# Kernel optimization log

Measured on AMD Instinct MI355X. Metric: run time of the kernel, lower is better.

Reference implementation:

```python
import jax, jax.numpy as jnp
import numpy as np

HIDDEN = 1024
HEADS = 16
HEAD_DIM = HIDDEN // HEADS


def setup_inputs() -> dict:
    key = jax.random.key(0)
    ks = jax.random.split(key, 9)
    s = 1.0 / np.sqrt(HIDDEN)
    inp = {
        "x": jax.random.normal(ks[0], (2, 2048, HIDDEN), dtype=jnp.float32),
        "Wq": jax.random.uniform(ks[1], (HIDDEN, HIDDEN), jnp.float32, -s, s),
        "bq": jax.random.uniform(ks[2], (HIDDEN,), jnp.float32, -s, s),
        "Wk": jax.random.uniform(ks[3], (HIDDEN, HIDDEN), jnp.float32, -s, s),
        "bk": jax.random.uniform(ks[4], (HIDDEN,), jnp.float32, -s, s),
        "Wv": jax.random.uniform(ks[5], (HIDDEN, HIDDEN), jnp.float32, -s, s),
        "bv": jax.random.uniform(ks[6], (HIDDEN,), jnp.float32, -s, s),
        "Wo": jax.random.uniform(ks[7], (HIDDEN, HIDDEN), jnp.float32, -s, s),
        "bo": jax.random.uniform(ks[8], (HIDDEN,), jnp.float32, -s, s),
    }
    return inp


def reference(x, Wq, bq, Wk, bk, Wv, bv, Wo, bo):
    B, S, _ = x.shape
    # QKV projections; reshape to [B, H, S, D]
    def heads(t):
        return t.reshape(B, S, HEADS, HEAD_DIM).transpose(0, 2, 1, 3)
    q = heads(x @ Wq + bq)
    k = heads(x @ Wk + bk)
    v = heads(x @ Wv + bv)
    scale = 1.0 / np.sqrt(HEAD_DIM)
    scores = jnp.einsum('bhqd,bhkd->bhqk', q, k) * scale  # [B,H,S,S]
    attn = jax.nn.softmax(scores, axis=-1)
    out = jnp.einsum('bhqk,bhkd->bhqd', attn, v)  # [B,H,S,D]
    out = out.transpose(0, 2, 1, 3).reshape(B, S, HIDDEN)
    return out @ Wo + bo
```

## Files before the change

kernel.cpp:

```cpp
#include <hip/hip_runtime.h>
#include <math.h>


namespace {

constexpr int kHID = 1024;
constexpr int kNH  = 16;
constexpr int kHD  = 64;
constexpr int kSEQ = 2048;

constexpr float kQScale = 0.125f * 1.4426950408889634f;

typedef unsigned short ushortT;
typedef __attribute__((ext_vector_type(8))) short   bf16x8;
typedef __attribute__((ext_vector_type(4))) float   f32x4;
typedef __attribute__((ext_vector_type(4))) unsigned short u16x4;

#define MFMA(a, b, c) __builtin_amdgcn_mfma_f32_16x16x32_bf16((a), (b), (c), 0, 0, 0)
#define SBAR() __builtin_amdgcn_s_barrier()
#define WAITV0() asm volatile("s_waitcnt vmcnt(0)" ::: "memory")
#define WAITV3() asm volatile("s_waitcnt vmcnt(3)" ::: "memory")
#define WAITV4() asm volatile("s_waitcnt vmcnt(4)" ::: "memory")

typedef const __attribute__((address_space(1))) void GVoid;
typedef __attribute__((address_space(3))) void SVoid;

__device__ __forceinline__ void gload_lds16(const ushortT* g, ushortT* l) {
    __builtin_amdgcn_global_load_lds((GVoid*)g, (SVoid*)l, 16, 0, 0);
}

__device__ __forceinline__ ushortT f2bf(float f) {
    unsigned u = __builtin_bit_cast(unsigned, f);
    u += 0x7fffu + ((u >> 16) & 1u);
    return (ushortT)(u >> 16);
}

__device__ __forceinline__ unsigned cvt_pk_bf16(float a, float b) {
    unsigned r;
    asm("v_cvt_pk_bf16_f32 %0, %1, %2" : "=v"(r) : "v"(a), "v"(b));
    return r;
}

__device__ __forceinline__ float4 ld4f(const float* p) { return *reinterpret_cast<const float4*>(p); }

__global__ __launch_bounds__(256) void prep_kernel(
    const float* __restrict__ x, ushortT* __restrict__ xb,
    const float* __restrict__ W0, const float* __restrict__ W1,
    const float* __restrict__ W2, const float* __restrict__ W3,
    ushortT* __restrict__ WtAll) {
    __shared__ ushortT T[64 * 72];
    const int bx = blockIdx.x;
    const int tid = threadIdx.x;

    if (bx < 4096) {
        const size_t i = ((size_t)bx * 256 + tid) * 4;
        const float4 f = ld4f(&x[i]);
        u16x4 o = { f2bf(f.x), f2bf(f.y), f2bf(f.z), f2bf(f.w) };
        *reinterpret_cast<u16x4*>(&xb[i]) = o;
        return;
    }

    const int id2 = bx - 4096;
    const int z = id2 >> 8;
    const float* W = (z == 0) ? W0 : (z == 1) ? W1 : (z == 2) ? W2 : W3;
    ushortT* Wt = WtAll + (size_t)z * kHID * kHID;
    const int kb = ((id2 >> 4) & 15) * 64, nb = (id2 & 15) * 64;
    {
        const int kr = tid >> 2, nc = (tid & 3) * 16;
        #pragma unroll
        for (int i = 0; i < 16; i += 4) {
            const float4 f = ld4f(&W[(size_t)(kb + kr) * kHID + nb + nc + i]);
            T[kr * 72 + nc + i + 0] = f2bf(f.x);
            T[kr * 72 + nc + i + 1] = f2bf(f.y);
            T[kr * 72 + nc + i + 2] = f2bf(f.z);
            T[kr * 72 + nc + i + 3] = f2bf(f.w);
        }
    }
    __syncthreads();
    {
        const int nr = tid >> 2, kc = (tid & 3) * 16;
        ushortT tmp[16];
        #pragma unroll
        for (int i = 0; i < 16; ++i) tmp[i] = T[(kc + i) * 72 + nr];
        *reinterpret_cast<bf16x8*>(&Wt[(size_t)(nb + nr) * kHID + kb + kc]) =
            *reinterpret_cast<bf16x8*>(&tmp[0]);
        *reinterpret_cast<bf16x8*>(&Wt[(size_t)(nb + nr) * kHID + kb + kc + 8]) =
            *reinterpret_cast<bf16x8*>(&tmp[8]);
    }
}

__global__ __launch_bounds__(256, 4) void qkv_mfma_gemm(
    const ushortT* __restrict__ A, const ushortT* __restrict__ WtAll,
    const float* __restrict__ bq, const float* __restrict__ bk, const float* __restrict__ bv,
    ushortT* __restrict__ qkvb) {
    __shared__ ushortT As[2 * 4096];
    __shared__ ushortT Bs[2 * 4096];

    const int z = blockIdx.z;
    const ushortT* Bt = WtAll + (size_t)z * kHID * kHID;
    const float* bias = (z == 0) ? bq : (z == 1) ? bk : bv;
    ushortT* out = qkvb + (size_t)z * 2 * kNH * kSEQ * kHD;
    const float scale = (z == 0) ? kQScale : 1.0f;

    const int tid = threadIdx.x, wid = tid >> 6, lane = tid & 63;
    const int hi = lane >> 4, lo = lane & 15;
    const int wr = wid >> 1, wc = wid & 1;
    const int rowBase = blockIdx.y * 128, colBase = blockIdx.x * 128;
    const int sr = lane >> 2, sj = lane & 3;

    const f32x4 z4 = {0.f, 0.f, 0.f, 0.f};
    f32x4 acc[4][4];
    #pragma unroll
    for (int mi = 0; mi < 4; ++mi)
        #pragma unroll
        for (int ni = 0; ni < 4; ++ni) acc[mi][ni] = z4;

    auto STAGE = [&](int buf, int k0) {
        #pragma unroll
        for (int i = 0; i < 2; ++i) {
            const int chunk = wid * 2 + i;
            const int row = chunk * 16 + sr;
            const int c8 = 8 * (sj ^ (sr & 3));
            gload_lds16(&A [(size_t)(rowBase + row) * kHID + k0 + c8], &As[buf * 4096 + chunk * 512]);
            gload_lds16(&Bt[(size_t)(colBase + row) * kHID + k0 + c8], &Bs[buf * 4096 + chunk * 512]);
        }
    };

    STAGE(0, 0);

    for (int t = 0; t < kHID / 32; ++t) {
        const int cur = t & 1;
        if (t + 1 < kHID / 32) {
            STAGE(cur ^ 1, (t + 1) * 32);
            WAITV4();
        } else {
            WAITV0();
        }
        SBAR();

        __builtin_amdgcn_s_setprio(1);
        bf16x8 af[4], bfr[4];
        #pragma unroll
        for (int mi = 0; mi < 4; ++mi) {
            const int row = 64 * wr + 16 * mi + lo;
            af[mi] = *reinterpret_cast<const bf16x8*>(
                &As[cur * 4096 + row * 32 + 8 * (hi ^ (row & 3))]);
        }
        #pragma unroll
        for (int ni = 0; ni < 4; ++ni) {
            const int row = 64 * wc + 16 * ni + lo;
            bfr[ni] = *reinterpret_cast<const bf16x8*>(
                &Bs[cur * 4096 + row * 32 + 8 * (hi ^ (row & 3))]);
        }
        #pragma unroll
        for (int mi = 0; mi < 4; ++mi)
            #pragma unroll
            for (int ni = 0; ni < 4; ++ni)
                acc[mi][ni] = MFMA(af[mi], bfr[ni], acc[mi][ni]);
        __builtin_amdgcn_s_setprio(0);

        SBAR();
    }

    #pragma unroll
    for (int ni = 0; ni < 4; ++ni) {
        const int col = colBase + 64 * wc + 16 * ni + lo;
        const float bcol = bias[col];
        const int h = col >> 6, d = col & 63;
        #pragma unroll
        for (int mi = 0; mi < 4; ++mi)
            #pragma unroll
            for (int r = 0; r < 4; ++r) {
                const int m = rowBase + 64 * wr + 16 * mi + 4 * hi + r;
                const int b = m >> 11, s = m & (kSEQ - 1);
                const ushortT val = f2bf((acc[mi][ni][r] + bcol) * scale);
                if (z == 2)
                    out[(((size_t)b * kNH + h) * kHD + d) * kSEQ + s] = val;
                else
                    out[(((size_t)b * kNH + h) * kSEQ + s) * kHD + d] = val;
            }
    }
}

__global__ __launch_bounds__(256, 2) void out_mfma_gemm(
    const ushortT* __restrict__ A, const ushortT* __restrict__ Bt,
    const float* __restrict__ bias, float* __restrict__ out) {
    __shared__ ushortT As[2 * 2048];
    __shared__ ushortT Bs[2 * 4096];

    const int tid = threadIdx.x, wid = tid >> 6, lane = tid & 63;
    const int hi = lane >> 4, lo = lane & 15;
    const int wr = wid >> 1, wc = wid & 1;
    const int rowBase = blockIdx.y * 64, colBase = blockIdx.x * 128;
    const int sr = lane >> 2, sj = lane & 3;

    const f32x4 z4 = {0.f, 0.f, 0.f, 0.f};
    f32x4 acc[2][4];
    #pragma unroll
    for (int mi = 0; mi < 2; ++mi)
        #pragma unroll
        for (int ni = 0; ni < 4; ++ni) acc[mi][ni] = z4;

    auto STAGE = [&](int buf, int k0) {
        {
            const int chunk = wid;
            const int row = chunk * 16 + sr;
            const int c8 = 8 * (sj ^ (sr & 3));
            gload_lds16(&A[(size_t)(rowBase + row) * kHID + k0 + c8], &As[buf * 2048 + chunk * 512]);
        }
        #pragma unroll
        for (int i = 0; i < 2; ++i) {
            const int chunk = wid * 2 + i;
            const int row = chunk * 16 + sr;
            const int c8 = 8 * (sj ^ (sr & 3));
            gload_lds16(&Bt[(size_t)(colBase + row) * kHID + k0 + c8], &Bs[buf * 4096 + chunk * 512]);
        }
    };

    STAGE(0, 0);

    for (int t = 0; t < kHID / 32; ++t) {
        const int cur = t & 1;
        if (t + 1 < kHID / 32) {
            STAGE(cur ^ 1, (t + 1) * 32);
            WAITV3();
        } else {
            WAITV0();
        }
        SBAR();

        __builtin_amdgcn_s_setprio(1);
        bf16x8 af[2], bfr[4];
        #pragma unroll
        for (int mi = 0; mi < 2; ++mi) {
            const int row = 32 * wr + 16 * mi + lo;
            af[mi] = *reinterpret_cast<const bf16x8*>(
                &As[cur * 2048 + row * 32 + 8 * (hi ^ (row & 3))]);
        }
        #pragma unroll
        for (int ni = 0; ni < 4; ++ni) {
            const int row = 64 * wc + 16 * ni + lo;
            bfr[ni] = *reinterpret_cast<const bf16x8*>(
                &Bs[cur * 4096 + row * 32 + 8 * (hi ^ (row & 3))]);
        }
        #pragma unroll
        for (int mi = 0; mi < 2; ++mi)
            #pragma unroll
            for (int ni = 0; ni < 4; ++ni)
                acc[mi][ni] = MFMA(af[mi], bfr[ni], acc[mi][ni]);
        __builtin_amdgcn_s_setprio(0);

        SBAR();
    }

    #pragma unroll
    for (int ni = 0; ni < 4; ++ni) {
        const int col = colBase + 64 * wc + 16 * ni + lo;
        const float bcol = bias[col];
        #pragma unroll
        for (int mi = 0; mi < 2; ++mi)
            #pragma unroll
            for (int r = 0; r < 4; ++r) {
                const int m = rowBase + 32 * wr + 16 * mi + 4 * hi + r;
                out[(size_t)m * kHID + col] = acc[mi][ni][r] + bcol;
            }
    }
}

__global__ __launch_bounds__(256, 4) void flash_mfma_kernel(
    const ushortT* __restrict__ Qb, const ushortT* __restrict__ Kb,
    const ushortT* __restrict__ Vtg, ushortT* __restrict__ Ob) {
    __shared__ ushortT Ks[2][64 * 64];
    __shared__ ushortT Vs[2][64 * 64];

    const int tid = threadIdx.x, wid = tid >> 6, lane = tid & 63;
    const int hi = lane >> 4, lo = lane & 15;
    const int h = blockIdx.x;
    const int q0 = blockIdx.y * 64;
    const size_t headBase = ((size_t)blockIdx.z * kNH + h) * (size_t)(kSEQ * kHD);
    const ushortT* Kg = Kb + headBase;
    const ushortT* Vg = Vtg + headBase;

    bf16x8 qf[2];
    #pragma unroll
    for (int c = 0; c < 2; ++c)
        qf[c] = *reinterpret_cast<const bf16x8*>(
            &Qb[headBase + (size_t)(q0 + 16 * wid + lo) * kHD + 32 * c + 8 * hi]);

    const short one = (short)0x3F80;
    const bf16x8 ones = {one, one, one, one, one, one, one, one};

    const f32x4 z4 = {0.f, 0.f, 0.f, 0.f};
    f32x4 acc[4] = {z4, z4, z4, z4};
    f32x4 accL = z4;

    const int r8 = lane >> 3, jc = lane & 7;

    const int kap0 = 8 * (lo >> 2) + (lo & 3);
    const int sk = (lo & 3) | (((lo >> 2) & 1) << 2);
    const int kx0 = (8 * hi) ^ (sk << 3);
    const int kx1 = (32 + 8 * hi) ^ (sk << 3);
    const int sv = (lo & 3) | (((lo >> 3) & 1) << 2);

    auto STAGE = [&](int buf, int kv0) {
        #pragma unroll
        for (int i = 0; i < 2; ++i) {
            const int rowBase = (i * 4 + wid) * 8;
            const int row = rowBase + r8;
            const int s8 = (r8 & 3) | ((wid & 1) << 2);
            gload_lds16(&Kg[(size_t)(kv0 + row) * kHD + 8 * (jc ^ s8)], &Ks[buf][rowBase * 64]);
            gload_lds16(&Vg[(size_t)row * kSEQ + kv0 + 8 * (jc ^ s8)], &Vs[buf][rowBase * 64]);
        }
    };

    STAGE(0, 0);

    for (int t = 0; t < kSEQ / 64; ++t) {
        const int cur = t & 1;
        if (t + 1 < kSEQ / 64) {
            STAGE(cur ^ 1, (t + 1) * 64);
            WAITV4();
        } else {
            WAITV0();
        }
        SBAR();

        f32x4 sc[4];
        __builtin_amdgcn_s_setprio(1);
        #pragma unroll
        for (int f = 0; f < 4; ++f) {
            const int kap = kap0 + 4 * (f & 1) + 32 * (f >> 1);
            const bf16x8 kf0 = *reinterpret_cast<const bf16x8*>(&Ks[cur][kap * 64 + kx0]);
            const bf16x8 kf1 = *reinterpret_cast<const bf16x8*>(&Ks[cur][kap * 64 + kx1]);
            sc[f] = MFMA(kf1, qf[1], MFMA(kf0, qf[0], z4));
        }
        __builtin_amdgcn_s_setprio(0);

        float p[4][4];
        #pragma unroll
        for (int f = 0; f < 4; ++f)
            #pragma unroll
            for (int r = 0; r < 4; ++r) p[f][r] = exp2f(sc[f][r]);

        union U { unsigned u[4]; bf16x8 v; };
        U pa0, pa1;
        pa0.u[0] = cvt_pk_bf16(p[0][0], p[0][1]);
        pa0.u[1] = cvt_pk_bf16(p[0][2], p[0][3]);
        pa0.u[2] = cvt_pk_bf16(p[1][0], p[1][1]);
        pa0.u[3] = cvt_pk_bf16(p[1][2], p[1][3]);
        pa1.u[0] = cvt_pk_bf16(p[2][0], p[2][1]);
        pa1.u[1] = cvt_pk_bf16(p[2][2], p[2][3]);
        pa1.u[2] = cvt_pk_bf16(p[3][0], p[3][1]);
        pa1.u[3] = cvt_pk_bf16(p[3][2], p[3][3]);

        __builtin_amdgcn_s_setprio(1);
        accL = MFMA(pa0.v, ones, accL);
        accL = MFMA(pa1.v, ones, accL);
        #pragma unroll
        for (int n = 0; n < 4; ++n) {
            const int vrow = 16 * n + lo;
            const bf16x8 vf0 = *reinterpret_cast<const bf16x8*>(
                &Vs[cur][vrow * 64 + ((8 * hi) ^ (sv << 3))]);
            const bf16x8 vf1 = *reinterpret_cast<const bf16x8*>(
                &Vs[cur][vrow * 64 + ((32 + 8 * hi) ^ (sv << 3))]);
            acc[n] = MFMA(pa0.v, vf0, acc[n]);
            acc[n] = MFMA(pa1.v, vf1, acc[n]);
        }
        __builtin_amdgcn_s_setprio(0);

        SBAR();
    }

    #pragma unroll
    for (int r = 0; r < 4; ++r) {
        const float inv = 1.0f / accL[r];
        const int s = q0 + 16 * wid + 4 * hi + r;
        const size_t base = ((size_t)blockIdx.z * kSEQ + s) * kHID + (size_t)h * kHD;
        #pragma unroll
        for (int n = 0; n < 4; ++n)
            Ob[base + 16 * n + lo] = f2bf(acc[n][r] * inv);
    }
}

}

extern "C" void kernel_launch(void* const* d_in, const int* in_sizes, int n_in,
                              void* d_out, int out_size, void* d_ws, size_t ws_size,
                              hipStream_t stream) {
    (void)in_sizes; (void)n_in; (void)out_size;
    const float* x  = (const float*)d_in[0];
    const float* Wq = (const float*)d_in[1];
    const float* bq = (const float*)d_in[2];
    const float* Wk = (const float*)d_in[3];
    const float* bk = (const float*)d_in[4];
    const float* Wv = (const float*)d_in[5];
    const float* bv = (const float*)d_in[6];
    const float* Wo = (const float*)d_in[7];
    const float* bo = (const float*)d_in[8];

    constexpr size_t kXE = (size_t)2 * kSEQ * kHID;
    constexpr size_t kWE = (size_t)kHID * kHID;
    const size_t needed = (kXE + 4 * kWE + 3 * kXE + kXE) * sizeof(ushortT);
    if (ws_size < needed) return;

    ushortT* xb    = (ushortT*)d_ws;
    ushortT* WtAll = xb + kXE;
    ushortT* qkvb  = WtAll + 4 * kWE;
    ushortT* attnb = qkvb + 3 * kXE;

    const ushortT* qb  = qkvb;
    const ushortT* kb  = qkvb + kXE;
    const ushortT* vtb = qkvb + 2 * kXE;

    prep_kernel<<<dim3(4096 + 4 * 256), 256, 0, stream>>>(
        x, xb, Wq, Wk, Wv, Wo, WtAll);

    qkv_mfma_gemm<<<dim3(8, 32, 3), 256, 0, stream>>>(xb, WtAll, bq, bk, bv, qkvb);

    flash_mfma_kernel<<<dim3(kNH, kSEQ / 64, 2), 256, 0, stream>>>(qb, kb, vtb, attnb);

    out_mfma_gemm<<<dim3(8, 64), 256, 0, stream>>>(attnb, WtAll + 3 * kWE, bo, (float*)d_out);
}
```

Measured before the change: 126.8 us.

## Switch flash attention to 32x32x16 MFMA with split-KV waves and LDS reduction

Result: slower. 131.3 us (+3.5%).

```diff
diff --git a/kernel.cpp b/kernel.cpp
--- a/kernel.cpp
+++ b/kernel.cpp
@@ -12,11 +12,13 @@
 constexpr float kQScale = 0.125f * 1.4426950408889634f;
 
 typedef unsigned short ushortT;
-typedef __attribute__((ext_vector_type(8))) short   bf16x8;
-typedef __attribute__((ext_vector_type(4))) float   f32x4;
-typedef __attribute__((ext_vector_type(4))) unsigned short u16x4;
-
-#define MFMA(a, b, c) __builtin_amdgcn_mfma_f32_16x16x32_bf16((a), (b), (c), 0, 0, 0)
+typedef __attribute__((ext_vector_type(8)))  short bf16x8;
+typedef __attribute__((ext_vector_type(4)))  float f32x4;
+typedef __attribute__((ext_vector_type(16))) float f32x16;
+typedef __attribute__((ext_vector_type(4)))  unsigned short u16x4;
+
+#define MFMA(a, b, c)   __builtin_amdgcn_mfma_f32_16x16x32_bf16((a), (b), (c), 0, 0, 0)
+#define MFMA32(a, b, c) __builtin_amdgcn_mfma_f32_32x32x16_bf16((a), (b), (c), 0, 0, 0)
 #define SBAR() __builtin_amdgcn_s_barrier()
 #define WAITV0() asm volatile("s_waitcnt vmcnt(0)" ::: "memory")
 #define WAITV3() asm volatile("s_waitcnt vmcnt(3)" ::: "memory")
@@ -274,46 +276,45 @@
     __shared__ ushortT Vs[2][64 * 64];
 
     const int tid = threadIdx.x, wid = tid >> 6, lane = tid & 63;
-    const int hi = lane >> 4, lo = lane & 15;
+    const int l31 = lane & 31, h5 = lane >> 5, l7 = lane & 7;
+    const int qh = wid & 1;
+    const int slab = wid >> 1;
     const int h = blockIdx.x;
     const int q0 = blockIdx.y * 64;
     const size_t headBase = ((size_t)blockIdx.z * kNH + h) * (size_t)(kSEQ * kHD);
     const ushortT* Kg = Kb + headBase;
     const ushortT* Vg = Vtg + headBase;
 
-    bf16x8 qf[2];
+    bf16x8 qf[4];
     #pragma unroll
-    for (int c = 0; c < 2; ++c)
+    for (int c = 0; c < 4; ++c)
         qf[c] = *reinterpret_cast<const bf16x8*>(
-            &Qb[headBase + (size_t)(q0 + 16 * wid + lo) * kHD + 32 * c + 8 * hi]);
+            &Qb[headBase + (size_t)(q0 + 32 * qh + l31) * kHD + 16 * c + 8 * h5]);
 
     const short one = (short)0x3F80;
     const bf16x8 ones = {one, one, one, one, one, one, one, one};
 
-    const f32x4 z4 = {0.f, 0.f, 0.f, 0.f};
-    f32x4 acc[4] = {z4, z4, z4, z4};
-    f32x4 accL = z4;
+    f32x16 acc0 = {};
+    f32x16 acc1 = {};
+    f32x16 lacc = {};
 
     const int r8 = lane >> 3, jc = lane & 7;
-
-    const int kap0 = 8 * (lo >> 2) + (lo & 3);
-    const int sk = (lo & 3) | (((lo >> 2) & 1) << 2);
-    const int kx0 = (8 * hi) ^ (sk << 3);
-    const int kx1 = (32 + 8 * hi) ^ (sk << 3);
-    const int sv = (lo & 3) | (((lo >> 3) & 1) << 2);
 
     auto STAGE = [&](int buf, int kv0) {
         #pragma unroll
         for (int i = 0; i < 2; ++i) {
             const int rowBase = (i * 4 + wid) * 8;
             const int row = rowBase + r8;
-            const int s8 = (r8 & 3) | ((wid & 1) << 2);
-            gload_lds16(&Kg[(size_t)(kv0 + row) * kHD + 8 * (jc ^ s8)], &Ks[buf][rowBase * 64]);
-            gload_lds16(&Vg[(size_t)row * kSEQ + kv0 + 8 * (jc ^ s8)], &Vs[buf][rowBase * 64]);
+            const int ksrc = (row & ~12) | ((row & 4) << 1) | ((row & 8) >> 1);
+            const int c8 = 8 * (jc ^ r8);
+            gload_lds16(&Kg[(size_t)(kv0 + ksrc) * kHD + c8], &Ks[buf][rowBase * 64]);
+            gload_lds16(&Vg[(size_t)row * kSEQ + kv0 + c8],   &Vs[buf][rowBase * 64]);
         }
     };
 
     STAGE(0, 0);
+
+    const int krowBase = (32 * slab + l31) * 64;
 
     for (int t = 0; t < kSEQ / 64; ++t) {
         const int cur = t & 1;
@@ -325,60 +326,72 @@
         }
         SBAR();
 
-        f32x4 sc[4];
+        f32x16 sc = {};
         __builtin_amdgcn_s_setprio(1);
         #pragma unroll
-        for (int f = 0; f < 4; ++f) {
-            const int kap = kap0 + 4 * (f & 1) + 32 * (f >> 1);
-            const bf16x8 kf0 = *reinterpret_cast<const bf16x8*>(&Ks[cur][kap * 64 + kx0]);
-            const bf16x8 kf1 = *reinterpret_cast<const bf16x8*>(&Ks[cur][kap * 64 + kx1]);
-            sc[f] = MFMA(kf1, qf[1], MFMA(kf0, qf[0], z4));
+        for (int c = 0; c < 4; ++c) {
+            const bf16x8 kf = *reinterpret_cast<const bf16x8*>(
+                &Ks[cur][krowBase + 8 * ((2 * c + h5) ^ l7)]);
+            sc = MFMA32(kf, qf[c], sc);
         }
         __builtin_amdgcn_s_setprio(0);
 
-        float p[4][4];
-        #pragma unroll
-        for (int f = 0; f < 4; ++f)
-            #pragma unroll
-            for (int r = 0; r < 4; ++r) p[f][r] = exp2f(sc[f][r]);
+        float p[16];
+        #pragma unroll
+        for (int j = 0; j < 16; ++j) p[j] = exp2f(sc[j]);
 
         union U { unsigned u[4]; bf16x8 v; };
         U pa0, pa1;
-        pa0.u[0] = cvt_pk_bf16(p[0][0], p[0][1]);
-        pa0.u[1] = cvt_pk_bf16(p[0][2], p[0][3]);
-        pa0.u[2] = cvt_pk_bf16(p[1][0], p[1][1]);
-        pa0.u[3] = cvt_pk_bf16(p[1][2], p[1][3]);
-        pa1.u[0] = cvt_pk_bf16(p[2][0], p[2][1]);
-        pa1.u[1] = cvt_pk_bf16(p[2][2], p[2][3]);
-        pa1.u[2] = cvt_pk_bf16(p[3][0], p[3][1]);
-        pa1.u[3] = cvt_pk_bf16(p[3][2], p[3][3]);
+        #pragma unroll
+        for (int j = 0; j < 4; ++j) {
+            pa0.u[j] = cvt_pk_bf16(p[2 * j],     p[2 * j + 1]);
+            pa1.u[j] = cvt_pk_bf16(p[8 + 2 * j], p[9 + 2 * j]);
+        }
 
         __builtin_amdgcn_s_setprio(1);
-        accL = MFMA(pa0.v, ones, accL);
-        accL = MFMA(pa1.v, ones, accL);
-        #pragma unroll
-        for (int n = 0; n < 4; ++n) {
-            const int vrow = 16 * n + lo;
+        lacc = MFMA32(pa0.v, ones, lacc);
+        lacc = MFMA32(pa1.v, ones, lacc);
+        #pragma unroll
+        for (int dt = 0; dt < 2; ++dt) {
+            const int vrowBase = (32 * dt + l31) * 64;
             const bf16x8 vf0 = *reinterpret_cast<const bf16x8*>(
-                &Vs[cur][vrow * 64 + ((8 * hi) ^ (sv << 3))]);
+                &Vs[cur][vrowBase + 8 * ((4 * slab + h5) ^ l7)]);
             const bf16x8 vf1 = *reinterpret_cast<const bf16x8*>(
-                &Vs[cur][vrow * 64 + ((32 + 8 * hi) ^ (sv << 3))]);
-            acc[n] = MFMA(pa0.v, vf0, acc[n]);
-            acc[n] = MFMA(pa1.v, vf1, acc[n]);
+                &Vs[cur][vrowBase + 8 * ((4 * slab + 2 + h5) ^ l7)]);
+            f32x16& a = dt ? acc1 : acc0;
+            a = MFMA32(pa0.v, vf0, a);
+            a = MFMA32(pa1.v, vf1, a);
         }
         __builtin_amdgcn_s_setprio(0);
 
         SBAR();
     }
 
-    #pragma unroll
-    for (int r = 0; r < 4; ++r) {
-        const float inv = 1.0f / accL[r];
-        const int s = q0 + 16 * wid + 4 * hi + r;
-        const size_t base = ((size_t)blockIdx.z * kSEQ + s) * kHID + (size_t)h * kHD;
-        #pragma unroll
-        for (int n = 0; n < 4; ++n)
-            Ob[base + 16 * n + lo] = f2bf(acc[n][r] * inv);
+    float* MO = reinterpret_cast<float*>(&Ks[0][0]);
+    float* ML = reinterpret_cast<float*>(&Vs[0][0]);
+
+    if (slab == 1) {
+        #pragma unroll
+        for (int r = 0; r < 16; ++r) {
+            const int qr = (r & 3) + 8 * (r >> 2) + 4 * h5;
+            MO[(qh * 32 + qr) * 64 + l31]      = acc0[r];
+            MO[(qh * 32 + qr) * 64 + 32 + l31] = acc1[r];
+            if (l31 == 0) ML[qh * 32 + qr] = lacc[r];
+        }
+    }
+    __syncthreads();
+    if (slab == 0) {
+        #pragma unroll
+        for (int r = 0; r < 16; ++r) {
+            const int qr = (r & 3) + 8 * (r >> 2) + 4 * h5;
+            const float o0 = acc0[r] + MO[(qh * 32 + qr) * 64 + l31];
+            const float o1 = acc1[r] + MO[(qh * 32 + qr) * 64 + 32 + l31];
+            const float inv = 1.0f / (lacc[r] + ML[qh * 32 + qr]);
+            const int q = q0 + 32 * qh + qr;
+            const size_t base = ((size_t)blockIdx.z * kSEQ + q) * kHID + (size_t)h * kHD;
+            Ob[base + l31]      = f2bf(o0 * inv);
+            Ob[base + 32 + l31] = f2bf(o1 * inv);
+        }
     }
 }
 
```
